# Kernel optimization log

Measured on AMD Instinct MI355X. Metric: run time of the kernel, lower is better.

## Reference

```python
import jax, jax.numpy as jnp
import numpy as np
from jax import lax

DILATIONS = (1, 3, 9, 27, 81, 1)
C = 128        # model channels
UP = 2048      # up-projection channels
K = 512        # filterbank kernel size
NZ = 64        # non_zero_elements kept by sparsify
B = 2
N = 32768      # n_samples


def conv1d(x, w, b, dilation=1, padding='VALID'):
    # x: [B,Cin,T], w: [Cout,Cin,Kw]
    y = lax.conv_general_dilated(x, w, (1,), padding, rhs_dilation=(dilation,),
                                 dimension_numbers=('NCH', 'OIH', 'NCH'))
    return y if b is None else y + b[None, :, None]


def dilated_stack(x, ws, bs, causal_past):
    # residual stack of kernel-2 dilated causal convs; 'only-past' pads left, 'only-future' pads right
    for i, d in enumerate(DILATIONS):
        pad = ((0, 0), (0, 0), (d, 0)) if causal_past else ((0, 0), (0, 0), (0, d))
        h = conv1d(jnp.pad(x, pad), ws[i], bs[i], dilation=d)
        x = x + jax.nn.leaky_relu(h, 0.2)
    return x


def sparsify_topk(x, k):
    # keep top-k values (soft=True: keep magnitudes) over flattened (C,T) per sample
    b = x.shape[0]
    flat = x.reshape(b, -1)
    vals, idx = lax.top_k(flat, k)
    out = jnp.zeros_like(flat).at[jnp.arange(b)[:, None], idx].set(vals)
    return out.reshape(x.shape)


def setup_inputs() -> dict:
    key = jax.random.key(0)
    ks = jax.random.split(key, 11)
    s = 0.1  # weight_init
    return {
        'x': jax.random.normal(ks[0], (B, 1, N), jnp.float32),
        'fb': jax.random.normal(ks[1], (C, 1, K), jnp.float32) * s,        # filterbank
        'enc_w': jax.random.normal(ks[2], (6, C, C, 2), jnp.float32) * s,
        'enc_b': jnp.zeros((6, C), jnp.float32),
        'up_w': jax.random.normal(ks[3], (UP, C, 1), jnp.float32) * s,
        'up_b': jnp.zeros((UP,), jnp.float32),
        'down_w': jax.random.normal(ks[4], (C, UP, 1), jnp.float32) * s,
        'down_b': jnp.zeros((C,), jnp.float32),
        'dec_w': jax.random.normal(ks[5], (6, C, C, 2), jnp.float32) * s,
        'dec_b': jnp.zeros((6, C), jnp.float32),
    }


def reference(x, fb, enc_w, enc_b, up_w, up_b, down_w, down_b, dec_w, dec_b):
    # filterbank analysis: [B,1,N] -> [B,C,N]
    spec = conv1d(x, fb, None, 1, ((K // 2, K // 2 - 1),))
    enc = dilated_stack(spec, enc_w, enc_b, causal_past=False)  # 'only-future'
    enc = conv1d(enc, up_w, up_b)            # [B,2048,N]
    enc = sparsify_topk(enc, NZ)             # 64 nonzeros per sample
    enc = conv1d(enc, down_w, down_b)        # [B,128,N]
    dec = dilated_stack(enc, dec_w, dec_b, causal_past=True)    # 'only-past'
    dec = jnp.pad(dec, ((0, 0), (0, 0), (0, 1)))                # F.pad(decoded, (0,1))
    # transposed convolve back to waveform: flipped filterbank, sum over channels
    kt = jnp.flip(fb, -1).transpose(1, 0, 2)  # [1,C,K]
    final = conv1d(dec, kt, None, 1, ((K // 2 - 1, K // 2),))[:, :, :N]
    return final
```

## Files before the change

### kernel.cpp

```cpp
#include <hip/hip_runtime.h>
#include <stdint.h>

#define NB  2
#define NC  128
#define NT  32768
#define KFB 512
#define NUP 2048
#define CAP 14336

typedef unsigned int u32;
typedef unsigned short u16;
typedef short s16;
typedef float f32x4 __attribute__((ext_vector_type(4)));
typedef s16 short8 __attribute__((ext_vector_type(8)));
typedef u32 u32x4 __attribute__((ext_vector_type(4)));

__device__ __forceinline__ u32 f2key(float v){
  u32 u = __float_as_uint(v);
  return (u & 0x80000000u) ? ~u : (u | 0x80000000u);
}
__device__ __forceinline__ float key2f(u32 k){
  u32 u = (k & 0x80000000u) ? (k & 0x7FFFFFFFu) : ~k;
  return __uint_as_float(u);
}
__device__ __forceinline__ u16 bf16rn(float v){
  u32 u = __float_as_uint(v);
  return (u16)((u + 0x7FFFu + ((u>>16)&1u)) >> 16);
}
__device__ __forceinline__ u32 packhl(float v){
  u16 h = bf16rn(v);
  u16 lo = bf16rn(v - __uint_as_float(((u32)h)<<16));
  return ((u32)h<<16) | lo;
}
__device__ __forceinline__ void unpack8(const u32* p, short8& xh, short8& xl){
  u32x4 r0 = *(const u32x4*)p;
  u32x4 r1 = *(const u32x4*)(p + 4);
  union { u32 u[4]; short8 v; } H, L;
  H.u[0] = __builtin_amdgcn_perm(r0.y, r0.x, 0x07060302u);
  H.u[1] = __builtin_amdgcn_perm(r0.w, r0.z, 0x07060302u);
  H.u[2] = __builtin_amdgcn_perm(r1.y, r1.x, 0x07060302u);
  H.u[3] = __builtin_amdgcn_perm(r1.w, r1.z, 0x07060302u);
  L.u[0] = __builtin_amdgcn_perm(r0.y, r0.x, 0x05040100u);
  L.u[1] = __builtin_amdgcn_perm(r0.w, r0.z, 0x05040100u);
  L.u[2] = __builtin_amdgcn_perm(r1.y, r1.x, 0x05040100u);
  L.u[3] = __builtin_amdgcn_perm(r1.w, r1.z, 0x05040100u);
  xh = H.v; xl = L.v;
}

#define RS 132

__global__ void k_init(u32* __restrict__ h1, u32* __restrict__ h2, int* __restrict__ counts){
  int i = blockIdx.x*256 + threadIdx.x;
  if (i < 2048) h1[i] = 0u;
  else if (i < 4096) h2[i-2048] = 0u;
  if (i < NB) counts[i] = 0;
}

__global__ __launch_bounds__(256) void k_prep(const float* __restrict__ encw,
    const float* __restrict__ decw, const float* __restrict__ upw,
    const float* __restrict__ fbw,
    u16* __restrict__ wdil, u16* __restrict__ wup, u16* __restrict__ wfb){
  int g = blockIdx.x*256 + threadIdx.x;
  if (g < 49152){
    int l = g & 63, mt = (g>>6)&7, s = (g>>9)&7, layer = g>>12;
    const float* W = (layer < 6) ? (encw + (size_t)layer*NC*NC*2)
                                 : (decw + (size_t)(layer-6)*NC*NC*2);
    int co = mt*16 + (l & 15);
    int kb = s*32 + ((l>>4)<<3);
    union { u16 h[8]; u32x4 q; } H, L;
    #pragma unroll
    for (int j=0;j<8;++j){
      int k = kb + j;
      float v = W[((size_t)co*NC + (k&127))*2 + (k>>7)];
      u16 h = bf16rn(v);
      H.h[j] = h;
      L.h[j] = bf16rn(v - __uint_as_float(((u32)h)<<16));
    }
    int unit = g >> 6;
    *(u32x4*)(wdil + (size_t)unit*1024 + (l<<3)) = H.q;
    *(u32x4*)(wdil + (size_t)unit*1024 + 512 + (l<<3)) = L.q;
  } else if (g < 81920){
    int g2 = g - 49152;
    int l = g2 & 63, umt = (g2>>6)&127, s = g2>>13;
    int u = umt*16 + (l & 15);
    int kb = s*32 + ((l>>4)<<3);
    union { u16 h[8]; u32x4 q; } H, L;
    #pragma unroll
    for (int j=0;j<8;++j){
      float v = upw[(size_t)u*NC + kb + j];
      u16 h = bf16rn(v);
      H.h[j] = h;
      L.h[j] = bf16rn(v - __uint_as_float(((u32)h)<<16));
    }
    int unit = g2 >> 6;
    *(u32x4*)(wup + (size_t)unit*1024 + (l<<3)) = H.q;
    *(u32x4*)(wup + (size_t)unit*1024 + 512 + (l<<3)) = L.q;
  } else if (g < 90112){
    int g3 = g - 81920;
    int l = g3 & 63, mt = (g3>>6)&7, s = g3>>9;
    int c = mt*16 + (l & 15);
    int kb = s*32 + ((l>>4)<<3);
    union { u16 h[8]; u32x4 q; } H, L;
    #pragma unroll
    for (int j=0;j<8;++j){
      float v = fbw[(size_t)c*KFB + kb + j];
      u16 h = bf16rn(v);
      H.h[j] = h;
      L.h[j] = bf16rn(v - __uint_as_float(((u32)h)<<16));
    }
    int unit = g3 >> 6;
    *(u32x4*)(wfb + (size_t)unit*1024 + (l<<3)) = H.q;
    *(u32x4*)(wfb + (size_t)unit*1024 + 512 + (l<<3)) = L.q;
  }
}

__global__ __launch_bounds__(256) void k_fb(const float* __restrict__ x,
    const u16* __restrict__ wfb, float* __restrict__ spec){
  __shared__ u32 xw[640];
  const int tid = threadIdx.x;
  const int t0 = blockIdx.x << 7;
  const int b  = blockIdx.y;
  const int lane = tid & 63, w = tid >> 6;
  const int wy = w >> 1, wx = w & 1;
  const int quad = lane >> 4, l15 = lane & 15;
  for (int i = tid; i < 640; i += 256){
    int t = t0 - 256 + i;
    float v = ((u32)t < (u32)NT) ? x[b*NT + t] : 0.0f;
    xw[i] = packhl(v);
  }
  __syncthreads();
  f32x4 acc[4][4] = {};
  for (int s = 0; s < 16; ++s){
    short8 ah[4], al[4];
    #pragma unroll
    for (int mt=0; mt<4; ++mt){
      const u16* p = wfb + (size_t)(s*8 + wy*4 + mt)*1024 + (lane<<3);
      ah[mt] = *(const short8*)p;
      al[mt] = *(const short8*)(p + 512);
    }
    short8 xh[4], xl[4];
    #pragma unroll
    for (int nt=0; nt<4; ++nt){
      int base = s*32 + quad*8 + (wx<<6) + (nt<<4) + l15;
      u32 r[8];
      #pragma unroll
      for (int j=0;j<8;++j) r[j] = xw[base + j];
      union { u32 u[4]; short8 v; } H, L;
      H.u[0] = __builtin_amdgcn_perm(r[1], r[0], 0x07060302u);
      H.u[1] = __builtin_amdgcn_perm(r[3], r[2], 0x07060302u);
      H.u[2] = __builtin_amdgcn_perm(r[5], r[4], 0x07060302u);
      H.u[3] = __builtin_amdgcn_perm(r[7], r[6], 0x07060302u);
      L.u[0] = __builtin_amdgcn_perm(r[1], r[0], 0x05040100u);
      L.u[1] = __builtin_amdgcn_perm(r[3], r[2], 0x05040100u);
      L.u[2] = __builtin_amdgcn_perm(r[5], r[4], 0x05040100u);
      L.u[3] = __builtin_amdgcn_perm(r[7], r[6], 0x05040100u);
      xh[nt] = H.v; xl[nt] = L.v;
    }
    #pragma unroll
    for (int mt=0; mt<4; ++mt){
      #pragma unroll
      for (int nt=0; nt<4; ++nt){
        acc[mt][nt] = __builtin_amdgcn_mfma_f32_16x16x32_bf16(ah[mt], xh[nt], acc[mt][nt], 0,0,0);
        acc[mt][nt] = __builtin_amdgcn_mfma_f32_16x16x32_bf16(ah[mt], xl[nt], acc[mt][nt], 0,0,0);
        acc[mt][nt] = __builtin_amdgcn_mfma_f32_16x16x32_bf16(al[mt], xh[nt], acc[mt][nt], 0,0,0);
      }
    }
  }
  #pragma unroll
  for (int mt=0; mt<4; ++mt){
    #pragma unroll
    for (int r=0; r<4; ++r){
      const int c = (wy<<6) + (mt<<4) + (quad<<2) + r;
      float* po = spec + (size_t)(b*NC+c)*NT + t0 + (wx<<6) + l15;
      #pragma unroll
      for (int nt=0; nt<4; ++nt) po[nt<<4] = acc[mt][nt][r];
    }
  }
}

__global__ __launch_bounds__(512,2) void k_stack(const float* __restrict__ xin,
    float* __restrict__ xout, const u16* __restrict__ wf,
    const float* __restrict__ biases, int mode){
  extern __shared__ u32 lx[];
  const int tid = threadIdx.x;
  const int b  = blockIdx.y;
  const int T0 = blockIdx.x << 7;
  const int row0g = mode ? (T0 - 122) : T0;
  const int lane = tid & 63, w = tid >> 6;
  const int wm = w >> 2, wn = w & 3;
  const int quad = lane >> 4, l15 = lane & 15;
  {
    const float* xb = xin + (size_t)b*NC*NT;
    const int row = tid >> 1;
    const int ci0 = (tid & 1) << 6;
    const int tg = row0g + row;
    const bool ok = ((u32)tg < (u32)NT);
    const float* src = xb + (size_t)ci0*NT + tg;
    u32* dst = lx + row*RS + ci0;
    #pragma unroll
    for (int g=0; g<16; ++g){
      u32x4 q;
      #pragma unroll
      for (int k=0;k<4;++k){
        float v = ok ? src[(size_t)(g*4 + k)*NT] : 0.0f;
        q[k] = packhl(v);
      }
      *(u32x4*)(dst + g*4) = q;
    }
  }
  const int dils[6] = {1,3,9,27,81,1};
  #pragma unroll 1
  for (int l = 0; l < 6; ++l){
    const int d = dils[l];
    const int o0 = mode ? -d : 0;
    const int o1 = mode ? 0 : d;
    const u16* wl = wf + ((size_t)l << 16);
    __syncthreads();
    f32x4 acc[4][4] = {};
    #pragma unroll 1
    for (int s = 0; s < 8; ++s){
      short8 ah[4], al[4];
      #pragma unroll
      for (int mt=0;mt<4;++mt){
        const u16* p = wl + (size_t)(((s<<3) + (wm<<2) + mt) << 10) + (lane<<3);
        ah[mt] = *(const short8*)p;
        al[mt] = *(const short8*)(p + 512);
      }
      const int o = (s >= 4) ? o1 : o0;
      const int cig = (s & 3) << 5;
      #pragma unroll
      for (int nt=0;nt<4;++nt){
        const int T = ((wn<<6) + (nt<<4) + l15 + o) & 255;
        const int idx = T*RS + cig + (quad<<3);
        short8 xh, xl;
        unpack8(&lx[idx], xh, xl);
        #pragma unroll
        for (int mt=0;mt<4;++mt){
          acc[mt][nt] = __builtin_amdgcn_mfma_f32_16x16x32_bf16(ah[mt], xh, acc[mt][nt], 0,0,0);
          acc[mt][nt] = __builtin_amdgcn_mfma_f32_16x16x32_bf16(ah[mt], xl, acc[mt][nt], 0,0,0);
          acc[mt][nt] = __builtin_amdgcn_mfma_f32_16x16x32_bf16(al[mt], xh, acc[mt][nt], 0,0,0);
        }
      }
    }
    __syncthreads();
    const float* bl = biases + l*NC;
    const bool last = (l == 5);
    #pragma unroll
    for (int mt=0;mt<4;++mt){
      const int cobase = (wm<<6) + (mt<<4) + (quad<<2);
      float bv[4];
      #pragma unroll
      for (int r=0;r<4;++r) bv[r] = bl[cobase + r];
      #pragma unroll
      for (int nt=0;nt<4;++nt){
        const int T = (wn<<6) + (nt<<4) + l15;
        const int idx = T*RS + cobase;
        u32x4 xo = *(const u32x4*)&lx[idx];
        const int tg = row0g + T;
        const bool tv = ((u32)tg < (u32)NT);
        float nv[4];
        #pragma unroll
        for (int r=0;r<4;++r){
          float oldv = __uint_as_float(xo[r] & 0xFFFF0000u) + __uint_as_float(xo[r] << 16);
          float h = acc[mt][nt][r] + bv[r];
          h = (h >= 0.f) ? h : 0.2f*h;
          float xn = oldv + h;
          nv[r] = tv ? xn : 0.0f;
        }
        if (!last){
          u32x4 np;
          #pragma unroll
          for (int r=0;r<4;++r) np[r] = packhl(nv[r]);
          *(u32x4*)&lx[idx] = np;
        } else {
          const bool rowok = mode ? (T >= 122 && T < 250) : (T < 128);
          if (rowok){
            float* po = xout + (size_t)(b*NC + cobase)*NT + tg;
            #pragma unroll
            for (int r=0;r<4;++r) po[(size_t)r*NT] = nv[r];
          }
        }
      }
    }
  }
}

__global__ __launch_bounds__(256) void k_sub(const float* __restrict__ enc,
                                             const float* __restrict__ upw,
                                             const float* __restrict__ upb,
                                             u32* __restrict__ keys,
                                             u32* __restrict__ hist1){
  const int u0 = blockIdx.x * 64;
  const int i0 = blockIdx.y * 256;
  const int b  = blockIdx.z;
  __shared__ float uwl[32][68];
  __shared__ float ec[32][260];
  __shared__ u32 lh[1024];
  const int tid = threadIdx.x;
  for (int i=tid;i<1024;i+=256) lh[i] = 0u;
  const int ug = tid & 15;
  const int ig = tid >> 4;
  float acc[4][16];
  #pragma unroll
  for (int i=0;i<4;++i){
    #pragma unroll
    for (int j=0;j<16;++j) acc[i][j]=0.0f;
  }
  for (int c0=0;c0<NC;c0+=32){
    __syncthreads();
    #pragma unroll
    for (int i=0;i<8;++i){
      int flat = i*256+tid;
      uwl[flat & 31][flat >> 5] = upw[(size_t)(u0 + (flat>>5))*NC + c0 + (flat&31)];
    }
    #pragma unroll
    for (int i=0;i<32;++i){
      int flat = i*256+tid;
      ec[flat >> 8][flat & 255] = enc[(size_t)(b*NC + c0 + (flat>>8))*NT + (size_t)(i0 + (flat&255))*32];
    }
    __syncthreads();
    #pragma unroll 2
    for (int cc=0;cc<32;++cc){
      float a[4], bb[16];
      *(float4*)&a[0] = *(const float4*)&uwl[cc][ug*4];
      #pragma unroll
      for (int m=0;m<4;++m)
        *(float4*)&bb[m*4] = *(const float4*)&ec[cc][ig*16 + m*4];
      #pragma unroll
      for (int i=0;i<4;++i){
        #pragma unroll
        for (int j=0;j<16;++j)
          acc[i][j] = fmaf(a[i], bb[j], acc[i][j]);
      }
    }
  }
  #pragma unroll
  for (int i=0;i<4;++i){
    int u = u0 + ug*4 + i;
    float ub = upb[u];
    #pragma unroll
    for (int j=0;j<16;++j){
      float v = acc[i][j] + ub;
      u32 k = f2key(v);
      keys[(size_t)(b*NUP + u)*1024 + i0 + ig*16 + j] = k;
      atomicAdd(&lh[k >> 22], 1u);
    }
  }
  __syncthreads();
  for (int i=tid;i<1024;i+=256){
    u32 c = lh[i];
    if (c) atomicAdd(&hist1[b*1024 + i], c);
  }
}

__global__ __launch_bounds__(256) void k_sel(const u32* __restrict__ hist,
                                             u32* __restrict__ cstar,
                                             u32* __restrict__ nab,
                                             u32* __restrict__ t0key,
                                             int phase){
  const int b = blockIdx.x;
  __shared__ u32 s1[1024];
  __shared__ u32 s2[1024];
  __shared__ int red[256];
  const int tid = threadIdx.x;
  for (int i=tid;i<1024;i+=256) s1[i] = hist[b*1024 + i];
  __syncthreads();
  u32* cur = s1; u32* nxt = s2;
  for (int off=1; off<1024; off<<=1){
    for (int i=tid;i<1024;i+=256){
      u32 v = cur[i];
      if (i + off < 1024) v += cur[i+off];
      nxt[i] = v;
    }
    __syncthreads();
    u32* t = cur; cur = nxt; nxt = t;
  }
  u32 off0 = (phase==1) ? 0u : nab[b];
  int best = -1;
  for (int i=tid;i<1024;i+=256)
    if (off0 + cur[i] >= 64u && i > best) best = i;
  red[tid] = best;
  __syncthreads();
  for (int st=128; st>0; st>>=1){
    if (tid < st) red[tid] = max(red[tid], red[tid+st]);
    __syncthreads();
  }
  if (tid == 0){
    int bi = (red[0] < 0) ? 0 : red[0];
    if (phase == 1){
      cstar[b] = (u32)bi;
      nab[b] = (bi < 1023) ? cur[bi+1] : 0u;
    } else {
      t0key[b] = (cstar[b] << 22) | (((u32)bi) << 12);
    }
  }
}

__global__ void k_h2(const u32* __restrict__ keys, const u32* __restrict__ cstar,
                     u32* __restrict__ hist2){
  const u32 c0 = cstar[0], c1 = cstar[1];
  int i = blockIdx.x*256 + threadIdx.x;
  const int total = NB*NUP*1024;
  const int stride = gridDim.x*256;
  for (; i < total; i += stride){
    u32 k = keys[i];
    u32 cs = (i >> 21) ? c1 : c0;
    if ((k >> 22) == cs) atomicAdd(&hist2[((u32)(i>>21)<<10) + ((k>>12) & 1023u)], 1u);
  }
}

__global__ __launch_bounds__(256,2) void k_up(const float* __restrict__ enc,
    const u16* __restrict__ wf, const float* __restrict__ upb,
    const u32* __restrict__ t0key, float* __restrict__ cval,
    int* __restrict__ cidx, int* __restrict__ counts){
  extern __shared__ u32 lx[];
  const int tid = threadIdx.x;
  const int t0 = blockIdx.x << 7;
  const int b  = blockIdx.y;
  const int lane = tid & 63, w = tid >> 6;
  const int wy = w >> 1, wx = w & 1;
  const int quad = lane >> 4, l15 = lane & 15;
  {
    const float* xb = enc + (size_t)b*NC*NT + t0;
    const int row = tid >> 1;
    const int ci0 = (tid & 1) << 6;
    const float* src = xb + (size_t)ci0*NT + row;
    u32* dst = lx + row*RS + ci0;
    #pragma unroll
    for (int g=0; g<16; ++g){
      u32x4 q;
      #pragma unroll
      for (int k=0;k<4;++k) q[k] = packhl(src[(size_t)(g*4 + k)*NT]);
      *(u32x4*)(dst + g*4) = q;
    }
  }
  __syncthreads();
  float T0 = key2f(t0key[b]);
  T0 -= fabsf(T0)*3e-4f + 1e-5f;
  #pragma unroll 1
  for (int uc = 0; uc < 16; ++uc){
    f32x4 acc[4][4] = {};
    #pragma unroll 1
    for (int s = 0; s < 4; ++s){
      short8 ah[4], al[4];
      #pragma unroll
      for (int mt=0;mt<4;++mt){
        const u16* p = wf + (size_t)((s*128 + uc*8 + wy*4 + mt) << 10) + (lane<<3);
        ah[mt] = *(const short8*)p;
        al[mt] = *(const short8*)(p + 512);
      }
      const int cig = s << 5;
      #pragma unroll
      for (int nt=0;nt<4;++nt){
        const int T = (wx<<6) + (nt<<4) + l15;
        short8 xh, xl;
        unpack8(&lx[T*RS + cig + (quad<<3)], xh, xl);
        #pragma unroll
        for (int mt=0;mt<4;++mt){
          acc[mt][nt] = __builtin_amdgcn_mfma_f32_16x16x32_bf16(ah[mt], xh, acc[mt][nt], 0,0,0);
          acc[mt][nt] = __builtin_amdgcn_mfma_f32_16x16x32_bf16(ah[mt], xl, acc[mt][nt], 0,0,0);
          acc[mt][nt] = __builtin_amdgcn_mfma_f32_16x16x32_bf16(al[mt], xh, acc[mt][nt], 0,0,0);
        }
      }
    }
    #pragma unroll
    for (int mt=0; mt<4; ++mt){
      #pragma unroll
      for (int r=0; r<4; ++r){
        int u = uc*128 + (wy<<6) + (mt<<4) + (quad<<2) + r;
        float ub = upb[u];
        #pragma unroll
        for (int nt=0; nt<4; ++nt){
          float v = acc[mt][nt][r] + ub;
          if (v >= T0){
            int slot = atomicAdd(&counts[b], 1);
            if (slot < CAP){
              cval[b*CAP + slot] = v;
              cidx[b*CAP + slot] = u*NT + (t0 + (wx<<6) + (nt<<4) + l15);
            }
          }
        }
      }
    }
  }
}

__global__ __launch_bounds__(256) void k_top(const float* __restrict__ cval,
                                             const int* __restrict__ cidx,
                                             const int* __restrict__ counts,
                                             float* __restrict__ tv,
                                             int* __restrict__ ti){
  const int b = blockIdx.x;
  __shared__ float lv[CAP];
  __shared__ float sv[256];
  __shared__ int   si[256];
  const int tid = threadIdx.x;
  int n = counts[b]; if (n > CAP) n = CAP;
  for (int i=tid;i<n;i+=256) lv[i] = cval[b*CAP+i];
  __syncthreads();
  for (int r=0;r<64;++r){
    float best = -3.4e38f; int bi = -1;
    for (int i=tid;i<n;i+=256){
      float v = lv[i];
      if (v > best){ best = v; bi = i; }
    }
    sv[tid]=best; si[tid]=bi;
    __syncthreads();
    for (int st=128; st>0; st>>=1){
      if (tid < st && sv[tid+st] > sv[tid]){ sv[tid]=sv[tid+st]; si[tid]=si[tid+st]; }
      __syncthreads();
    }
    if (tid == 0){
      int kb = si[0];
      if (kb >= 0){
        tv[b*64+r] = sv[0];
        ti[b*64+r] = cidx[b*CAP+kb];
        lv[kb] = -3.4e38f;
      } else { tv[b*64+r] = 0.0f; ti[b*64+r] = 0; }
    }
    __syncthreads();
  }
}

__global__ void k_fill(float* __restrict__ dst, const float* __restrict__ downb){
  const int bc = blockIdx.x;
  const int c = bc & 127;
  float v = downb[c];
  float4 vv; vv.x=v; vv.y=v; vv.z=v; vv.w=v;
  float4* p = (float4*)(dst + (size_t)bc*NT);
  for (int i=threadIdx.x; i < NT/4; i += 256) p[i] = vv;
}

__global__ void k_scat(float* __restrict__ dst, const float* __restrict__ downw,
                       const float* __restrict__ tv, const int* __restrict__ ti){
  const int b = blockIdx.x, r = blockIdx.y;
  float v = tv[b*64+r];
  int idx = ti[b*64+r];
  int u = idx / NT, t = idx - u*NT;
  int c = threadIdx.x;
  atomicAdd(&dst[(size_t)(b*NC+c)*NT + t], downw[(size_t)c*NUP + u] * v);
}

#define TS 4096
__global__ __launch_bounds__(256) void k_syn(const float* __restrict__ dec,
                                             const float* __restrict__ fb,
                                             float* __restrict__ part){
  const int ts = blockIdx.x;
  const int cs = blockIdx.y;
  const int b  = blockIdx.z;
  const int t0 = ts * TS;
  __shared__ float win2[16*289 + 8];
  __shared__ float fbl[512];
  const int tid = threadIdx.x;
  const int tl = tid * 16;
  float acc[16];
  #pragma unroll
  for (int j=0;j<16;++j) acc[j] = 0.0f;
  for (int c = cs*4; c < cs*4+4; ++c){
    __syncthreads();
    for (int i=tid; i < TS+511; i += 256){
      int t = t0 - 255 + i;
      win2[(i & 15)*289 + (i >> 4)] = ((u32)t < (u32)NT) ? dec[(size_t)(b*NC+c)*NT + t] : 0.0f;
    }
    for (int i=tid; i<512; i+=256) fbl[i] = fb[c*KFB + i];
    __syncthreads();
    float w[23];
    #pragma unroll
    for (int k=0;k<23;++k){
      int i = tl + 504 + k;
      w[k] = win2[(i & 15)*289 + (i >> 4)];
    }
    for (int G=0; G<64; ++G){
      float4 f0 = *(const float4*)&fbl[G*8];
      float4 f1 = *(const float4*)&fbl[G*8+4];
      float fq[8] = {f0.x, f0.y, f0.z, f0.w, f1.x, f1.y, f1.z, f1.w};
      #pragma unroll
      for (int q=0;q<8;++q){
        #pragma unroll
        for (int jj=0;jj<16;++jj)
          acc[jj] = fmaf(fq[q], w[7-q+jj], acc[jj]);
      }
      if (G != 63){
        #pragma unroll
        for (int k=22;k>=8;--k) w[k] = w[k-8];
        #pragma unroll
        for (int k=0;k<8;++k){
          int i = tl + 496 - 8*G + k;
          w[k] = win2[(i & 15)*289 + (i >> 4)];
        }
      }
    }
  }
  float* po = &part[(size_t)(cs*NB + b)*NT + t0 + tl];
  #pragma unroll
  for (int m=0;m<4;++m){
    float4 ov; ov.x=acc[m*4+0]; ov.y=acc[m*4+1]; ov.z=acc[m*4+2]; ov.w=acc[m*4+3];
    *(float4*)&po[m*4] = ov;
  }
}

__global__ void k_red(const float* __restrict__ part, float* __restrict__ out){
  int i = blockIdx.x*256 + threadIdx.x;
  float s = 0.0f;
  #pragma unroll
  for (int cs=0;cs<32;++cs) s += part[(size_t)cs*(NB*NT) + i];
  out[i] = s;
}

extern "C" void kernel_launch(void* const* d_in, const int* in_sizes, int n_in,
                              void* d_out, int out_size, void* d_ws, size_t ws_size,
                              hipStream_t stream){
  const float* x    = (const float*)d_in[0];
  const float* fb   = (const float*)d_in[1];
  const float* encw = (const float*)d_in[2];
  const float* encb = (const float*)d_in[3];
  const float* upw  = (const float*)d_in[4];
  const float* upb  = (const float*)d_in[5];
  const float* dnw  = (const float*)d_in[6];
  const float* dnb  = (const float*)d_in[7];
  const float* decw = (const float*)d_in[8];
  const float* decb = (const float*)d_in[9];
  float* out = (float*)d_out;
  char* ws = (char*)d_ws;

  size_t o = 0;
  float* bufA = (float*)(ws + o); o += (size_t)NB*NC*NT*4;
  float* bufB = (float*)(ws + o); o += (size_t)NB*NC*NT*4;
  u32*  keys  = (u32*)(ws + o);   o += (size_t)NB*NUP*1024*4;
  u32*  hist1 = (u32*)(ws + o);   o += 1024*NB*4;
  u32*  hist2 = (u32*)(ws + o);   o += 1024*NB*4;
  u32*  cstar = (u32*)(ws + o);   o += 64;
  u32*  nab   = (u32*)(ws + o);   o += 64;
  u32*  t0k   = (u32*)(ws + o);   o += 64;
  int*  cnt   = (int*)(ws + o);   o += 64;
  float* tv   = (float*)(ws + o); o += NB*64*4;
  int*  ti    = (int*)(ws + o);   o += NB*64*4;
  float* cval = (float*)(ws + o); o += (size_t)NB*CAP*4;
  int*  cidx  = (int*)(ws + o);   o += (size_t)NB*CAP*4;
  u16*  wdil  = (u16*)(ws + o);   o += (size_t)12*65536*2;
  u16*  wup   = (u16*)(ws + o);   o += (size_t)4*128*1024*2;
  u16*  wfb   = (u16*)(ws + o);   o += (size_t)128*1024*2;
  float* part = (float*)keys;

  k_init<<<dim3(16), dim3(256), 0, stream>>>(hist1, hist2, cnt);
  k_prep<<<dim3(352), dim3(256), 0, stream>>>(encw, decw, upw, fb, wdil, wup, wfb);
  k_fb<<<dim3(256,NB), dim3(256), 0, stream>>>(x, wfb, bufA);

  k_stack<<<dim3(256,NB), dim3(512), 256*RS*4, stream>>>(bufA, bufB, wdil, encb, 0);

  k_sub<<<dim3(32,4,NB), dim3(256), 0, stream>>>(bufB, upw, upb, keys, hist1);
  k_sel<<<dim3(NB), dim3(256), 0, stream>>>(hist1, cstar, nab, t0k, 1);
  k_h2 <<<dim3(4096), dim3(256), 0, stream>>>(keys, cstar, hist2);
  k_sel<<<dim3(NB), dim3(256), 0, stream>>>(hist2, cstar, nab, t0k, 2);
  k_up <<<dim3(256,NB), dim3(256), 128*RS*4, stream>>>(bufB, wup, upb, t0k, cval, cidx, cnt);
  k_top<<<dim3(NB), dim3(256), 0, stream>>>(cval, cidx, cnt, tv, ti);

  k_fill<<<dim3(NB*NC), dim3(256), 0, stream>>>(bufA, dnb);
  k_scat<<<dim3(NB,64), dim3(128), 0, stream>>>(bufA, dnw, tv, ti);

  k_stack<<<dim3(256,NB), dim3(512), 256*RS*4, stream>>>(bufA, bufB, wdil + (size_t)6*65536, decb, 1);

  k_syn<<<dim3(8,32,NB), dim3(256), 0, stream>>>(bufB, fb, part);
  k_red<<<dim3(256), dim3(256), 0, stream>>>(part, out);
}
```

Baseline: 864.5 us.

## Widen stack blocks, skip halo tiles, register top-k, split synthesis further

k_stack now runs 1024 threads per block, with each wave covering 2 output-channel tiles instead of 4. Per layer it skips the time tiles outside the halo region still needed by later layers, which removes redundant MFMA work on the receptive-field overlap. k_top keeps candidates in registers and uses wavefront shuffle reductions when there are at most 4096 candidates, replacing the shared-memory tree reduction. The synthesis kernel splits channels into 64 groups instead of 32 for more parallelism, at the cost of more partial sums for k_red to add, and k_init is folded into k_prep to save a launch.

```diff
diff --git a/kernel.cpp b/kernel.cpp
--- a/kernel.cpp
+++ b/kernel.cpp
@@ -49,18 +49,15 @@
 
 #define RS 132
 
-__global__ void k_init(u32* __restrict__ h1, u32* __restrict__ h2, int* __restrict__ counts){
-  int i = blockIdx.x*256 + threadIdx.x;
-  if (i < 2048) h1[i] = 0u;
-  else if (i < 4096) h2[i-2048] = 0u;
-  if (i < NB) counts[i] = 0;
-}
-
 __global__ __launch_bounds__(256) void k_prep(const float* __restrict__ encw,
     const float* __restrict__ decw, const float* __restrict__ upw,
     const float* __restrict__ fbw,
-    u16* __restrict__ wdil, u16* __restrict__ wup, u16* __restrict__ wfb){
+    u16* __restrict__ wdil, u16* __restrict__ wup, u16* __restrict__ wfb,
+    u32* __restrict__ h1, u32* __restrict__ h2, int* __restrict__ counts){
   int g = blockIdx.x*256 + threadIdx.x;
+  if (g < 2048) h1[g] = 0u;
+  else if (g < 4096) h2[g-2048] = 0u;
+  if (g < NB) counts[g] = 0;
   if (g < 49152){
     int l = g & 63, mt = (g>>6)&7, s = (g>>9)&7, layer = g>>12;
     const float* W = (layer < 6) ? (encw + (size_t)layer*NC*NC*2)
@@ -178,7 +175,7 @@
   }
 }
 
-__global__ __launch_bounds__(512,2) void k_stack(const float* __restrict__ xin,
+__global__ __launch_bounds__(1024,4) void k_stack(const float* __restrict__ xin,
     float* __restrict__ xout, const u16* __restrict__ wf,
     const float* __restrict__ biases, int mode){
   extern __shared__ u32 lx[];
@@ -191,14 +188,14 @@
   const int quad = lane >> 4, l15 = lane & 15;
   {
     const float* xb = xin + (size_t)b*NC*NT;
-    const int row = tid >> 1;
-    const int ci0 = (tid & 1) << 6;
+    const int row = tid & 255;
+    const int ci0 = (tid >> 8) << 5;
     const int tg = row0g + row;
     const bool ok = ((u32)tg < (u32)NT);
     const float* src = xb + (size_t)ci0*NT + tg;
     u32* dst = lx + row*RS + ci0;
     #pragma unroll
-    for (int g=0; g<16; ++g){
+    for (int g=0; g<8; ++g){
       u32x4 q;
       #pragma unroll
       for (int k=0;k<4;++k){
@@ -209,20 +206,29 @@
     }
   }
   const int dils[6] = {1,3,9,27,81,1};
+  const int Hrem[6] = {121,118,109,82,1,0};
   #pragma unroll 1
   for (int l = 0; l < 6; ++l){
     const int d = dils[l];
     const int o0 = mode ? -d : 0;
     const int o1 = mode ? 0 : d;
+    const int lo = mode ? (122 - Hrem[l]) : 0;
+    const int hi = mode ? 250 : (128 + Hrem[l]);
     const u16* wl = wf + ((size_t)l << 16);
     __syncthreads();
-    f32x4 acc[4][4] = {};
+    bool act[4];
+    #pragma unroll
+    for (int nt=0;nt<4;++nt){
+      const int Tst = (wn<<6) + (nt<<4);
+      act[nt] = (Tst + 16 > lo) && (Tst < hi);
+    }
+    f32x4 acc[2][4] = {};
     #pragma unroll 1
     for (int s = 0; s < 8; ++s){
-      short8 ah[4], al[4];
-      #pragma unroll
-      for (int mt=0;mt<4;++mt){
-        const u16* p = wl + (size_t)(((s<<3) + (wm<<2) + mt) << 10) + (lane<<3);
+      short8 ah[2], al[2];
+      #pragma unroll
+      for (int mt=0;mt<2;++mt){
+        const u16* p = wl + (size_t)(((s<<3) + (wm<<1) + mt) << 10) + (lane<<3);
         ah[mt] = *(const short8*)p;
         al[mt] = *(const short8*)(p + 512);
       }
@@ -230,12 +236,13 @@
       const int cig = (s & 3) << 5;
       #pragma unroll
       for (int nt=0;nt<4;++nt){
+        if (!act[nt]) continue;
         const int T = ((wn<<6) + (nt<<4) + l15 + o) & 255;
         const int idx = T*RS + cig + (quad<<3);
         short8 xh, xl;
         unpack8(&lx[idx], xh, xl);
         #pragma unroll
-        for (int mt=0;mt<4;++mt){
+        for (int mt=0;mt<2;++mt){
           acc[mt][nt] = __builtin_amdgcn_mfma_f32_16x16x32_bf16(ah[mt], xh, acc[mt][nt], 0,0,0);
           acc[mt][nt] = __builtin_amdgcn_mfma_f32_16x16x32_bf16(ah[mt], xl, acc[mt][nt], 0,0,0);
           acc[mt][nt] = __builtin_amdgcn_mfma_f32_16x16x32_bf16(al[mt], xh, acc[mt][nt], 0,0,0);
@@ -246,18 +253,19 @@
     const float* bl = biases + l*NC;
     const bool last = (l == 5);
     #pragma unroll
-    for (int mt=0;mt<4;++mt){
-      const int cobase = (wm<<6) + (mt<<4) + (quad<<2);
+    for (int mt=0;mt<2;++mt){
+      const int cobase = (wm<<5) + (mt<<4) + (quad<<2);
       float bv[4];
       #pragma unroll
       for (int r=0;r<4;++r) bv[r] = bl[cobase + r];
       #pragma unroll
       for (int nt=0;nt<4;++nt){
+        if (!act[nt]) continue;
         const int T = (wn<<6) + (nt<<4) + l15;
         const int idx = T*RS + cobase;
         u32x4 xo = *(const u32x4*)&lx[idx];
         const int tg = row0g + T;
-        const bool tv = ((u32)tg < (u32)NT);
+        const bool tvld = ((u32)tg < (u32)NT);
         float nv[4];
         #pragma unroll
         for (int r=0;r<4;++r){
@@ -265,7 +273,7 @@
           float h = acc[mt][nt][r] + bv[r];
           h = (h >= 0.f) ? h : 0.2f*h;
           float xn = oldv + h;
-          nv[r] = tv ? xn : 0.0f;
+          nv[r] = tvld ? xn : 0.0f;
         }
         if (!last){
           u32x4 np;
@@ -496,29 +504,64 @@
   __shared__ int   si[256];
   const int tid = threadIdx.x;
   int n = counts[b]; if (n > CAP) n = CAP;
-  for (int i=tid;i<n;i+=256) lv[i] = cval[b*CAP+i];
-  __syncthreads();
-  for (int r=0;r<64;++r){
-    float best = -3.4e38f; int bi = -1;
-    for (int i=tid;i<n;i+=256){
-      float v = lv[i];
-      if (v > best){ best = v; bi = i; }
-    }
-    sv[tid]=best; si[tid]=bi;
-    __syncthreads();
-    for (int st=128; st>0; st>>=1){
-      if (tid < st && sv[tid+st] > sv[tid]){ sv[tid]=sv[tid+st]; si[tid]=si[tid+st]; }
+  if (n <= 4096){
+    float v[16];
+    #pragma unroll
+    for (int r=0;r<16;++r){
+      int i = r*256 + tid;
+      v[r] = (i < n) ? cval[b*CAP+i] : -3.4e38f;
+    }
+    const int lane = tid & 63, wv = tid >> 6;
+    for (int r=0;r<64;++r){
+      float best = v[0]; int bidx = 0;
+      #pragma unroll
+      for (int k=1;k<16;++k){ if (v[k] > best){ best = v[k]; bidx = k; } }
+      int gi = bidx*256 + tid;
+      #pragma unroll
+      for (int off=32; off>0; off>>=1){
+        float ov = __shfl_down(best, off);
+        int oi = __shfl_down(gi, off);
+        if (ov > best){ best = ov; gi = oi; }
+      }
+      if (lane == 0){ sv[wv] = best; si[wv] = gi; }
       __syncthreads();
-    }
-    if (tid == 0){
-      int kb = si[0];
-      if (kb >= 0){
-        tv[b*64+r] = sv[0];
-        ti[b*64+r] = cidx[b*CAP+kb];
-        lv[kb] = -3.4e38f;
-      } else { tv[b*64+r] = 0.0f; ti[b*64+r] = 0; }
-    }
-    __syncthreads();
+      if (tid == 0){
+        float bb = sv[0]; int bbi = si[0];
+        #pragma unroll
+        for (int k=1;k<4;++k) if (sv[k] > bb){ bb = sv[k]; bbi = si[k]; }
+        si[4] = bbi;
+        if (bb > -3.0e38f){ tv[b*64+r] = bb; ti[b*64+r] = cidx[b*CAP + bbi]; }
+        else { tv[b*64+r] = 0.0f; ti[b*64+r] = 0; }
+      }
+      __syncthreads();
+      int wini = si[4];
+      if ((wini & 255) == tid) v[wini >> 8] = -3.4e38f;
+    }
+  } else {
+    for (int i=tid;i<n;i+=256) lv[i] = cval[b*CAP+i];
+    __syncthreads();
+    for (int r=0;r<64;++r){
+      float best = -3.4e38f; int bi = -1;
+      for (int i=tid;i<n;i+=256){
+        float v = lv[i];
+        if (v > best){ best = v; bi = i; }
+      }
+      sv[tid]=best; si[tid]=bi;
+      __syncthreads();
+      for (int st=128; st>0; st>>=1){
+        if (tid < st && sv[tid+st] > sv[tid]){ sv[tid]=sv[tid+st]; si[tid]=si[tid+st]; }
+        __syncthreads();
+      }
+      if (tid == 0){
+        int kb = si[0];
+        if (kb >= 0){
+          tv[b*64+r] = sv[0];
+          ti[b*64+r] = cidx[b*CAP+kb];
+          lv[kb] = -3.4e38f;
+        } else { tv[b*64+r] = 0.0f; ti[b*64+r] = 0; }
+      }
+      __syncthreads();
+    }
   }
 }
 
@@ -556,7 +599,7 @@
   float acc[16];
   #pragma unroll
   for (int j=0;j<16;++j) acc[j] = 0.0f;
-  for (int c = cs*4; c < cs*4+4; ++c){
+  for (int c = cs*2; c < cs*2+2; ++c){
     __syncthreads();
     for (int i=tid; i < TS+511; i += 256){
       int t = t0 - 255 + i;
@@ -603,7 +646,7 @@
   int i = blockIdx.x*256 + threadIdx.x;
   float s = 0.0f;
   #pragma unroll
-  for (int cs=0;cs<32;++cs) s += part[(size_t)cs*(NB*NT) + i];
+  for (int cs=0;cs<64;++cs) s += part[(size_t)cs*(NB*NT) + i];
   out[i] = s;
 }
 
@@ -642,11 +685,10 @@
   u16*  wfb   = (u16*)(ws + o);   o += (size_t)128*1024*2;
   float* part = (float*)keys;
 
-  k_init<<<dim3(16), dim3(256), 0, stream>>>(hist1, hist2, cnt);
-  k_prep<<<dim3(352), dim3(256), 0, stream>>>(encw, decw, upw, fb, wdil, wup, wfb);
+  k_prep<<<dim3(352), dim3(256), 0, stream>>>(encw, decw, upw, fb, wdil, wup, wfb, hist1, hist2, cnt);
   k_fb<<<dim3(256,NB), dim3(256), 0, stream>>>(x, wfb, bufA);
 
-  k_stack<<<dim3(256,NB), dim3(512), 256*RS*4, stream>>>(bufA, bufB, wdil, encb, 0);
+  k_stack<<<dim3(256,NB), dim3(1024), 256*RS*4, stream>>>(bufA, bufB, wdil, encb, 0);
 
   k_sub<<<dim3(32,4,NB), dim3(256), 0, stream>>>(bufB, upw, upb, keys, hist1);
   k_sel<<<dim3(NB), dim3(256), 0, stream>>>(hist1, cstar, nab, t0k, 1);
@@ -658,8 +700,8 @@
   k_fill<<<dim3(NB*NC), dim3(256), 0, stream>>>(bufA, dnb);
   k_scat<<<dim3(NB,64), dim3(128), 0, stream>>>(bufA, dnw, tv, ti);
 
-  k_stack<<<dim3(256,NB), dim3(512), 256*RS*4, stream>>>(bufA, bufB, wdil + (size_t)6*65536, decb, 1);
-
-  k_syn<<<dim3(8,32,NB), dim3(256), 0, stream>>>(bufB, fb, part);
+  k_stack<<<dim3(256,NB), dim3(1024), 256*RS*4, stream>>>(bufA, bufB, wdil + (size_t)6*65536, decb, 1);
+
+  k_syn<<<dim3(8,64,NB), dim3(256), 0, stream>>>(bufB, fb, part);
   k_red<<<dim3(256), dim3(256), 0, stream>>>(part, out);
 }
```

Result: faster. 819.5 us (-5.2%).
